# Performance work log

Measured on AMD Instinct MI355X. Metric: run time of the kernel, lower is better.

## Reference

```python
import jax, jax.numpy as jnp
import numpy as np


def _mha(q, k, v, num_heads):
    # q,k,v: [B, L, C] -> multi-head attention, scale = 1/sqrt(head_dim)
    B, Lq, C = q.shape
    Lk = k.shape[1]
    d = C // num_heads
    qh = q.reshape(B, Lq, num_heads, d)
    kh = k.reshape(B, Lk, num_heads, d)
    vh = v.reshape(B, Lk, num_heads, d)
    scale = 1.0 / jnp.sqrt(jnp.asarray(d, q.dtype))
    scores = jnp.einsum('blhd,bmhd->bhlm', qh, kh) * scale
    probs = jax.nn.softmax(scores, axis=-1)
    out = jnp.einsum('bhlm,bmhd->blhd', probs, vh)
    return out.reshape(B, Lq, C)


def setup_inputs() -> dict:
    key = jax.random.key(0)
    ks = jax.random.split(key, 9)
    b, n, f, l, C = 1, 4, 8, 256, 320
    s = 0.02
    return {
        'hidden_states': jax.random.normal(ks[0], (b * n * f, l, C), jnp.float32),
        'Wq': jax.random.normal(ks[1], (C, C), jnp.float32) * s,
        'Wk': jax.random.normal(ks[2], (C, C), jnp.float32) * s,
        'Wv': jax.random.normal(ks[3], (C, C), jnp.float32) * s,
        'Wo': jax.random.normal(ks[4], (C, C), jnp.float32) * s,
        'bo': jnp.zeros((C,), jnp.float32),
        'Wq_i2v': jax.random.normal(ks[5], (C, C), jnp.float32) * s,
        'Wo_i2v': jax.random.normal(ks[6], (C, C), jnp.float32) * s,
        'bo_i2v': jnp.zeros((C,), jnp.float32),
        'num_heads': 8,
        'num_views': 4,
        'num_frames': 8,
    }


def reference(hidden_states, Wq, Wk, Wv, Wo, bo, Wq_i2v, Wo_i2v, bo_i2v,
              num_heads, num_views, num_frames):
    BNF, l, C = hidden_states.shape
    n, f = num_views, num_frames
    b = BNF // (n * f)
    # '(b n f) l c -> (b f) (n l) c'
    h = hidden_states.reshape(b, n, f, l, C).transpose(0, 2, 1, 3, 4).reshape(b * f, n * l, C)
    L = n * l

    q = h @ Wq
    k = h @ Wk
    v = h @ Wv

    # first-frame KV broadcast across all frames within the same b
    k_first = jnp.broadcast_to(k.reshape(b, f, L, C)[:, 0:1], (b, f, L, C)).reshape(b * f, L, C)
    v_first = jnp.broadcast_to(v.reshape(b, f, L, C)[:, 0:1], (b, f, L, C)).reshape(b * f, L, C)

    base = _mha(q, k, v, num_heads)

    q_i2v = h @ Wq_i2v
    i2v = _mha(q_i2v, k_first, v_first, num_heads)
    i2v = i2v @ Wo_i2v + bo_i2v

    out = (base + i2v) @ Wo + bo

    # '(b f) (n l) c -> (b n f) l c'
    out = out.reshape(b, f, n, l, C).transpose(0, 2, 1, 3, 4).reshape(b * n * f, l, C)
    return out
```

## Files before the change

kernel.cpp:

```cpp
#include <hip/hip_runtime.h>

#define MROWS 8192
#define CDIM  320
#define QPAD  512

typedef __attribute__((ext_vector_type(8))) short bf16x8;
typedef __attribute__((ext_vector_type(4))) float f32x4;

__device__ __forceinline__ unsigned bfbits(float x) {
  union { float f; unsigned u; } a; a.f = x;
  return a.u + 0x8000u;
}
__device__ __forceinline__ unsigned pack2bf(float a, float b) {
  return (bfbits(a) >> 16) | (bfbits(b) & 0xffff0000u);
}
__device__ __forceinline__ void splitbf(float x, short& hi, short& lo) {
  unsigned hu = bfbits(x) & 0xffff0000u;
  union { unsigned u; float f; } h; h.u = hu;
  hi = (short)(hu >> 16);
  lo = (short)(bfbits(x - h.f) >> 16);
}

__device__ __forceinline__ int swizzle_row(int r) {
  int ff = r >> 10;
  int t  = r & 1023;
  int nn = t >> 8;
  int ll = t & 255;
  return nn * 2048 + ff * 256 + ll;
}

__global__ __launch_bounds__(256) void wc_kernel(
    const float* __restrict__ Woi, const float* __restrict__ Wo,
    float* __restrict__ Wc)
{
  const int r0 = blockIdx.x * 64, c0 = blockIdx.y * 64;
  __shared__ float As[64][36];
  __shared__ float Bs[32][68];
  const int tid = threadIdx.x, tx = tid & 15, ty = tid >> 4;
  float acc[4][4] = {};

  const int ra = tid >> 3, kq = (tid & 7) * 4;
  const int kb = tid >> 4, cq = (tid & 15) * 4;

  for (int k0 = 0; k0 < 320; k0 += 32) {
    float4 a1 = *(const float4*)(Woi + (size_t)(r0 + ra) * 320 + k0 + kq);
    float4 a2 = *(const float4*)(Woi + (size_t)(r0 + ra + 32) * 320 + k0 + kq);
    float4 b1 = *(const float4*)(Wo + (size_t)(k0 + kb) * 320 + c0 + cq);
    float4 b2 = *(const float4*)(Wo + (size_t)(k0 + kb + 16) * 320 + c0 + cq);
    __syncthreads();
    *(float4*)&As[ra][kq] = a1;
    *(float4*)&As[ra + 32][kq] = a2;
    *(float4*)&Bs[kb][cq] = b1;
    *(float4*)&Bs[kb + 16][cq] = b2;
    __syncthreads();
    #pragma unroll
    for (int kk = 0; kk < 32; ++kk) {
      float4 bv = *(const float4*)&Bs[kk][tx * 4];
      #pragma unroll
      for (int i = 0; i < 4; ++i) {
        float a = As[ty * 4 + i][kk];
        acc[i][0] = fmaf(a, bv.x, acc[i][0]);
        acc[i][1] = fmaf(a, bv.y, acc[i][1]);
        acc[i][2] = fmaf(a, bv.z, acc[i][2]);
        acc[i][3] = fmaf(a, bv.w, acc[i][3]);
      }
    }
  }
  #pragma unroll
  for (int i = 0; i < 4; ++i) {
    float4 v = make_float4(acc[i][0], acc[i][1], acc[i][2], acc[i][3]);
    *(float4*)(Wc + (size_t)(r0 + ty * 4 + i) * 320 + c0 + tx * 4) = v;
  }
}

__global__ __launch_bounds__(256) void pack_kernel(
    const float* __restrict__ hidden,
    const float* __restrict__ Wq, const float* __restrict__ Wk,
    const float* __restrict__ Wv, const float* __restrict__ Wqi,
    const float* __restrict__ Wo, const float* __restrict__ Wc,
    const float* __restrict__ bo, const float* __restrict__ boi,
    short* __restrict__ Ah, short* __restrict__ Al,
    short* __restrict__ WTh, short* __restrict__ WTl,
    short* __restrict__ WFh, short* __restrict__ WFl,
    float* __restrict__ bc,
    short* __restrict__ Qp, short* __restrict__ Kp, short* __restrict__ Qip,
    float qscale)
{
  const int b = blockIdx.x, tid = threadIdx.x;
  if (b < 64) {
    const int r0 = b * 128;
    for (int e = tid; e < 128 * 80; e += 256) {
      int r = e / 80, cq = (e % 80) * 4;
      float4 x = *(const float4*)(hidden + (size_t)swizzle_row(r0 + r) * 320 + cq);
      union { ushort4 v; short s[4]; } h, l;
      splitbf(x.x, h.s[0], l.s[0]); splitbf(x.y, h.s[1], l.s[1]);
      splitbf(x.z, h.s[2], l.s[2]); splitbf(x.w, h.s[3], l.s[3]);
      *(ushort4*)&Ah[(size_t)(r0 + r) * 320 + cq] = h.v;
      *(ushort4*)&Al[(size_t)(r0 + r) * 320 + cq] = l.v;
    }
  } else if (b < 128) {
    const int t2 = b - 64, wi = t2 >> 4, seg = t2 & 15;
    const float* W = wi == 0 ? Wq : wi == 1 ? Wk : wi == 2 ? Wv : Wqi;
    const float s = (wi == 0 || wi == 3) ? qscale : 1.0f;
    short* th = WTh + (size_t)wi * 320 * 320;
    short* tl = WTl + (size_t)wi * 320 * 320;
    for (int e = tid; e < 20 * 320; e += 256) {
      int n = seg * 20 + e / 320, k = e % 320;
      short hi, lo;
      splitbf(W[(size_t)k * 320 + n] * s, hi, lo);
      th[(size_t)n * 320 + k] = hi;
      tl[(size_t)n * 320 + k] = lo;
    }
  } else if (b < 160) {
    const int t2 = b - 128;
    for (int e = tid; e < 10 * 640; e += 256) {
      int n = t2 * 10 + e / 640, k = e % 640;
      float x = (k < 320) ? Wo[(size_t)k * 320 + n] : Wc[(size_t)(k - 320) * 320 + n];
      short hi, lo;
      splitbf(x, hi, lo);
      WFh[(size_t)n * 640 + k] = hi;
      WFl[(size_t)n * 640 + k] = lo;
    }
  } else if (b < 168) {
    const int n = (b - 160) * 40 + tid;
    if (tid < 40) {
      float s = bo[n];
      for (int j = 0; j < 320; ++j) s = fmaf(boi[j], Wo[(size_t)j * 320 + n], s);
      bc[n] = s;
    }
  } else {
    const int bz = b - 168, buf = bz >> 5, seg = bz & 31;
    short* P = buf == 0 ? Qp : buf == 1 ? Kp : Qip;
    const uint4 z = make_uint4(0, 0, 0, 0);
    for (int e = tid; e < 256 * 24; e += 256) {
      int row = (seg << 8) + (e / 24);
      int cc = e % 24, h = cc / 3, c3 = cc % 3;
      *(uint4*)&P[(size_t)row * QPAD + h * 64 + 40 + c3 * 8] = z;
    }
  }
}

__global__ __launch_bounds__(256, 3) void mfma_gemm(
    const short* __restrict__ Ah, const short* __restrict__ Al,
    const short* __restrict__ BTh, const short* __restrict__ BTl,
    int K, int mode,
    short* __restrict__ Qp, short* __restrict__ Kp,
    short* __restrict__ Vt, short* __restrict__ Qip,
    float* __restrict__ Of, const float* __restrict__ bias)
{
  const int tid  = threadIdx.x;
  const int wave = tid >> 6;
  const int lane = tid & 63;
  const int quad = lane >> 4;
  const int l16  = lane & 15;
  const int row0 = blockIdx.x * 128;

  const short *bth, *btl;
  int nbase, wi = 0;
  if (mode == 0) {
    const int ct = blockIdx.y;
    wi = ct / 5;
    bth = BTh + (size_t)wi * 320 * 320;
    btl = BTl + (size_t)wi * 320 * 320;
    nbase = (ct % 5) * 64;
  } else {
    bth = BTh; btl = BTl;
    nbase = blockIdx.y * 64;
  }

  __shared__ short Ash[128][40], Asl[128][40];
  __shared__ short Bsh[64][40],  Bsl[64][40];

  f32x4 acc[2][4];
  #pragma unroll
  for (int mt = 0; mt < 2; ++mt)
    #pragma unroll
    for (int nt = 0; nt < 4; ++nt) acc[mt][nt] = (f32x4){0.f, 0.f, 0.f, 0.f};

  const int ar = tid >> 2, akc = (tid & 3) * 8;
  const int bn = tid >> 2, bkc = (tid & 3) * 8;

  const short* pa_h = Ah + (size_t)(row0 + ar) * K + akc;
  const short* pa_l = Al ? Al + (size_t)(row0 + ar) * K + akc : nullptr;
  const short* pb_h = bth + (size_t)(nbase + bn) * K + bkc;
  const short* pb_l = btl + (size_t)(nbase + bn) * K + bkc;

  for (int k0 = 0; k0 < K; k0 += 32) {
    uint4 ah1 = *(const uint4*)(pa_h + k0);
    uint4 ah2 = *(const uint4*)(pa_h + (size_t)64 * K + k0);
    uint4 al1, al2;
    if (Al) {
      al1 = *(const uint4*)(pa_l + k0);
      al2 = *(const uint4*)(pa_l + (size_t)64 * K + k0);
    }
    uint4 bh = *(const uint4*)(pb_h + k0);
    uint4 bl = *(const uint4*)(pb_l + k0);
    __syncthreads();
    *(uint4*)&Ash[ar][akc]      = ah1;
    *(uint4*)&Ash[ar + 64][akc] = ah2;
    if (Al) {
      *(uint4*)&Asl[ar][akc]      = al1;
      *(uint4*)&Asl[ar + 64][akc] = al2;
    }
    *(uint4*)&Bsh[bn][bkc] = bh;
    *(uint4*)&Bsl[bn][bkc] = bl;
    __syncthreads();

    bf16x8 afh[2], afl[2], bfh[4], bfl[4];
    #pragma unroll
    for (int mt = 0; mt < 2; ++mt) {
      afh[mt] = *(const bf16x8*)&Ash[wave * 32 + mt * 16 + l16][quad * 8];
      if (Al) afl[mt] = *(const bf16x8*)&Asl[wave * 32 + mt * 16 + l16][quad * 8];
    }
    #pragma unroll
    for (int nt = 0; nt < 4; ++nt) {
      bfh[nt] = *(const bf16x8*)&Bsh[nt * 16 + l16][quad * 8];
      bfl[nt] = *(const bf16x8*)&Bsl[nt * 16 + l16][quad * 8];
    }
    #pragma unroll
    for (int mt = 0; mt < 2; ++mt)
      #pragma unroll
      for (int nt = 0; nt < 4; ++nt) {
        acc[mt][nt] = __builtin_amdgcn_mfma_f32_16x16x32_bf16(afh[mt], bfh[nt], acc[mt][nt], 0, 0, 0);
        acc[mt][nt] = __builtin_amdgcn_mfma_f32_16x16x32_bf16(afh[mt], bfl[nt], acc[mt][nt], 0, 0, 0);
        if (Al)
          acc[mt][nt] = __builtin_amdgcn_mfma_f32_16x16x32_bf16(afl[mt], bfh[nt], acc[mt][nt], 0, 0, 0);
      }
  }

  if (mode == 0) {
    if (wi == 2) {
      #pragma unroll
      for (int mt = 0; mt < 2; ++mt)
        #pragma unroll
        for (int nt = 0; nt < 4; ++nt) {
          const int col  = nbase + nt * 16 + l16;
          const int rowb = row0 + wave * 32 + mt * 16 + quad * 4;
          union { ushort4 v; short s[4]; } pk;
          #pragma unroll
          for (int r = 0; r < 4; ++r) pk.s[r] = (short)(bfbits(acc[mt][nt][r]) >> 16);
          *(ushort4*)&Vt[(size_t)col * MROWS + rowb] = pk.v;
        }
    } else {
      short* Op = wi == 0 ? Qp : wi == 1 ? Kp : Qip;
      #pragma unroll
      for (int mt = 0; mt < 2; ++mt)
        #pragma unroll
        for (int nt = 0; nt < 4; ++nt) {
          const int col  = nbase + nt * 16 + l16;
          const int h    = col / 40;
          const int pcol = h * 64 + (col - h * 40);
          const int rowb = row0 + wave * 32 + mt * 16 + quad * 4;
          #pragma unroll
          for (int r = 0; r < 4; ++r)
            Op[(size_t)(rowb + r) * QPAD + pcol] = (short)(bfbits(acc[mt][nt][r]) >> 16);
        }
    }
  } else {
    #pragma unroll
    for (int mt = 0; mt < 2; ++mt)
      #pragma unroll
      for (int nt = 0; nt < 4; ++nt) {
        const int col  = nbase + nt * 16 + l16;
        const int rowb = row0 + wave * 32 + mt * 16 + quad * 4;
        const float bb = bias[col];
        #pragma unroll
        for (int r = 0; r < 4; ++r)
          Of[(size_t)swizzle_row(rowb + r) * CDIM + col] = acc[mt][nt][r] + bb;
      }
  }
}

__global__ __launch_bounds__(64, 2) void attn_kernel(
    const short* __restrict__ Qp, const short* __restrict__ Qip,
    const short* __restrict__ Kp, const short* __restrict__ Vtg,
    short* __restrict__ AOh)
{
  const int qblk = blockIdx.x;
  const int hh   = blockIdx.y;
  const int zz   = blockIdx.z;
  const int var  = zz >> 3;
  const int bf   = zz & 7;
  const int lane = threadIdx.x;
  const int quad = lane >> 4;
  const int l16  = lane & 15;

  const short* Q = var ? Qip : Qp;
  const int kvbase = var ? 0 : (bf << 10);
  const int coff = var * 320 + hh * 40;

  __shared__ short Ps[4][16][72];

  bf16x8 qf0[4], qf1[4];
  #pragma unroll
  for (int qt = 0; qt < 4; ++qt) {
    const short* qp = Q + (size_t)((bf << 10) + (qblk << 6) + (qt << 4) + l16) * QPAD + hh * 64;
    qf0[qt] = *(const bf16x8*)(qp + quad * 8);
    qf1[qt] = *(const bf16x8*)(qp + 32 + quad * 8);
  }

  f32x4 acc[4][3];
  float lsum[4];
  #pragma unroll
  for (int qt = 0; qt < 4; ++qt) {
    lsum[qt] = 0.f;
    #pragma unroll
    for (int t = 0; t < 3; ++t) acc[qt][t] = (f32x4){0.f, 0.f, 0.f, 0.f};
  }

  const short* Kb = Kp + (size_t)kvbase * QPAD + hh * 64;
  const short* Vb = Vtg + (size_t)(hh * 40) * MROWS + kvbase;

  for (int s0 = 0; s0 < 1024; s0 += 64) {
    bf16x8 kb0[4], kb1[4];
    #pragma unroll
    for (int kt = 0; kt < 4; ++kt) {
      const short* kp = Kb + (size_t)(s0 + kt * 16 + l16) * QPAD;
      kb0[kt] = *(const bf16x8*)(kp + quad * 8);
      kb1[kt] = *(const bf16x8*)(kp + 32 + quad * 8);
    }

    #pragma unroll
    for (int qt = 0; qt < 4; ++qt) {
      float ls = 0.f;
      #pragma unroll
      for (int kt = 0; kt < 4; ++kt) {
        f32x4 st = (f32x4){0.f, 0.f, 0.f, 0.f};
        st = __builtin_amdgcn_mfma_f32_16x16x32_bf16(kb0[kt], qf0[qt], st, 0, 0, 0);
        st = __builtin_amdgcn_mfma_f32_16x16x32_bf16(kb1[kt], qf1[qt], st, 0, 0, 0);
        float p0 = __expf(st[0]);
        float p1 = __expf(st[1]);
        float p2 = __expf(st[2]);
        float p3 = __expf(st[3]);
        ls += (p0 + p1) + (p2 + p3);
        uint2 pk;
        pk.x = pack2bf(p0, p1);
        pk.y = pack2bf(p2, p3);
        *(uint2*)&Ps[qt][l16][kt * 16 + quad * 4] = pk;
      }
      lsum[qt] += ls;
    }

    asm volatile("s_waitcnt lgkmcnt(0)" ::: "memory");

    bf16x8 vf[2][3];
    #pragma unroll
    for (int kh = 0; kh < 2; ++kh)
      #pragma unroll
      for (int t = 0; t < 3; ++t)
        vf[kh][t] = *(const bf16x8*)(Vb + (size_t)(t * 16 + l16) * MROWS + s0 + kh * 32 + quad * 8);

    #pragma unroll
    for (int qt = 0; qt < 4; ++qt) {
      bf16x8 pa0 = *(const bf16x8*)&Ps[qt][l16][quad * 8];
      bf16x8 pa1 = *(const bf16x8*)&Ps[qt][l16][32 + quad * 8];
      #pragma unroll
      for (int t = 0; t < 3; ++t) {
        acc[qt][t] = __builtin_amdgcn_mfma_f32_16x16x32_bf16(pa0, vf[0][t], acc[qt][t], 0, 0, 0);
        acc[qt][t] = __builtin_amdgcn_mfma_f32_16x16x32_bf16(pa1, vf[1][t], acc[qt][t], 0, 0, 0);
      }
    }
  }

  #pragma unroll
  for (int qt = 0; qt < 4; ++qt) {
    float li = lsum[qt];
    li += __shfl_xor(li, 16);
    li += __shfl_xor(li, 32);
    float inv = 1.f / li;
    float invr[4];
    #pragma unroll
    for (int r = 0; r < 4; ++r) invr[r] = __shfl(inv, quad * 4 + r, 64);

    const int baserow = (bf << 10) + (qblk << 6) + (qt << 4) + quad * 4;
    #pragma unroll
    for (int t = 0; t < 3; ++t) {
      int dcol = t * 16 + l16;
      if (dcol < 40) {
        short* op = AOh + (size_t)baserow * 640 + coff + dcol;
        #pragma unroll
        for (int r = 0; r < 4; ++r)
          op[(size_t)r * 640] = (short)(bfbits(acc[qt][t][r] * invr[r]) >> 16);
      }
    }
  }
}

extern "C" void kernel_launch(void* const* d_in, const int* in_sizes, int n_in,
                              void* d_out, int out_size, void* d_ws, size_t ws_size,
                              hipStream_t stream) {
  const float* hidden  = (const float*)d_in[0];
  const float* Wq      = (const float*)d_in[1];
  const float* Wk      = (const float*)d_in[2];
  const float* Wv      = (const float*)d_in[3];
  const float* Wo      = (const float*)d_in[4];
  const float* bo      = (const float*)d_in[5];
  const float* Wq_i2v  = (const float*)d_in[6];
  const float* Wo_i2v  = (const float*)d_in[7];
  const float* bo_i2v  = (const float*)d_in[8];
  float* out = (float*)d_out;

  const size_t SZ  = (size_t)MROWS * CDIM;
  const size_t SZP = (size_t)MROWS * QPAD;
  short* Ah  = (short*)d_ws;
  short* Al  = Ah + SZ;
  short* AOh = Ah;
  short* Qp  = Al + SZ;
  short* Kp  = Qp + SZP;
  short* Qip = Kp + SZP;
  short* Vt  = Qip + SZP;
  short* WTh = Vt + (size_t)328 * MROWS;
  short* WTl = WTh + 409600;
  short* WFh = WTl + 409600;
  short* WFl = WFh + 204800;
  float* Wc  = (float*)(WFl + 204800);
  float* bc  = Wc + 102400;

  const float qscale = 0.15811388300841898f;

  wc_kernel<<<dim3(5, 5), 256, 0, stream>>>(Wo_i2v, Wo, Wc);

  pack_kernel<<<dim3(264), 256, 0, stream>>>(
      hidden, Wq, Wk, Wv, Wq_i2v, Wo, Wc, bo, bo_i2v,
      Ah, Al, WTh, WTl, WFh, WFl, bc, Qp, Kp, Qip, qscale);

  mfma_gemm<<<dim3(64, 20), 256, 0, stream>>>(
      Ah, Al, WTh, WTl, 320, 0, Qp, Kp, Vt, Qip, nullptr, nullptr);

  attn_kernel<<<dim3(16, 8, 16), 64, 0, stream>>>(Qp, Qip, Kp, Vt, AOh);

  mfma_gemm<<<dim3(64, 5), 256, 0, stream>>>(
      AOh, nullptr, WFh, WFl, 640, 1, nullptr, nullptr, nullptr, nullptr, out, bc);
}
```

Before: 229.2 us.

## Share K/V tiles in LDS across four waves per attention block

The attention kernel moves from one wave per 64-query block to four waves per 128-query block, each wave handling 32 queries. K and V tiles are staged cooperatively into shared memory once per key step and read by all four waves, instead of each wave loading them from global memory. The K rows are permuted through gbase so the reordered key columns line up with how P is packed. This adds two barriers per iteration and halves the number of blocks, which lowers latency hiding per block and makes the row permutation a correctness risk.

New measurement: 219.8 us. 4.1% less time.

```diff
diff --git a/kernel.cpp b/kernel.cpp
--- a/kernel.cpp
+++ b/kernel.cpp
@@ -271,7 +271,7 @@
   }
 }
 
-__global__ __launch_bounds__(64, 2) void attn_kernel(
+__global__ __launch_bounds__(256, 4) void attn_kernel(
     const short* __restrict__ Qp, const short* __restrict__ Qip,
     const short* __restrict__ Kp, const short* __restrict__ Vtg,
     short* __restrict__ AOh)
@@ -281,7 +281,9 @@
   const int zz   = blockIdx.z;
   const int var  = zz >> 3;
   const int bf   = zz & 7;
-  const int lane = threadIdx.x;
+  const int tid  = threadIdx.x;
+  const int wave = tid >> 6;
+  const int lane = tid & 63;
   const int quad = lane >> 4;
   const int l16  = lane & 15;
 
@@ -289,39 +291,63 @@
   const int kvbase = var ? 0 : (bf << 10);
   const int coff = var * 320 + hh * 40;
 
-  __shared__ short Ps[4][16][72];
-
-  bf16x8 qf0[4], qf1[4];
+  __shared__ short Ks[64][80];
+  __shared__ short Vt[48][72];
+  __shared__ short Ps[4][2][16][72];
+
+  if (tid < 64) {
+    *(uint4*)&Vt[40 + (tid >> 3)][(tid & 7) * 8] = make_uint4(0, 0, 0, 0);
+  }
+
+  bf16x8 qf0[2], qf1[2];
   #pragma unroll
-  for (int qt = 0; qt < 4; ++qt) {
-    const short* qp = Q + (size_t)((bf << 10) + (qblk << 6) + (qt << 4) + l16) * QPAD + hh * 64;
+  for (int qt = 0; qt < 2; ++qt) {
+    const short* qp = Q + (size_t)((bf << 10) + (qblk << 7) + (wave << 5) + (qt << 4) + l16) * QPAD + hh * 64;
     qf0[qt] = *(const bf16x8*)(qp + quad * 8);
     qf1[qt] = *(const bf16x8*)(qp + 32 + quad * 8);
   }
 
-  f32x4 acc[4][3];
-  float lsum[4];
+  f32x4 acc[2][3];
+  float lsum[2] = {0.f, 0.f};
   #pragma unroll
-  for (int qt = 0; qt < 4; ++qt) {
-    lsum[qt] = 0.f;
+  for (int qt = 0; qt < 2; ++qt)
     #pragma unroll
     for (int t = 0; t < 3; ++t) acc[qt][t] = (f32x4){0.f, 0.f, 0.f, 0.f};
-  }
 
   const short* Kb = Kp + (size_t)kvbase * QPAD + hh * 64;
   const short* Vb = Vtg + (size_t)(hh * 40) * MROWS + kvbase;
 
+  const int gbase = (l16 & 3) + ((l16 >> 2) << 4);
+
   for (int s0 = 0; s0 < 1024; s0 += 64) {
+    __syncthreads();
+    #pragma unroll
+    for (int pass = 0; pass < 4; ++pass) {
+      int u = tid + (pass << 8);
+      if (u < 512) {
+        int key = u >> 3, c = u & 7;
+        *(uint4*)&Ks[key][c * 8] =
+            *(const uint4*)(Kb + (size_t)(s0 + key) * QPAD + c * 8);
+      } else if (u < 832) {
+        int v = u - 512;
+        int dcol = v >> 3, ch = v & 7;
+        *(uint4*)&Vt[dcol][ch * 8] =
+            *(const uint4*)(Vb + (size_t)dcol * MROWS + s0 + ch * 8);
+      }
+    }
+    __syncthreads();
+
     bf16x8 kb0[4], kb1[4];
     #pragma unroll
     for (int kt = 0; kt < 4; ++kt) {
-      const short* kp = Kb + (size_t)(s0 + kt * 16 + l16) * QPAD;
-      kb0[kt] = *(const bf16x8*)(kp + quad * 8);
-      kb1[kt] = *(const bf16x8*)(kp + 32 + quad * 8);
-    }
-
-    #pragma unroll
-    for (int qt = 0; qt < 4; ++qt) {
+      const short* kr = &Ks[gbase + 4 * kt][quad * 8];
+      kb0[kt] = *(const bf16x8*)kr;
+      kb1[kt] = *(const bf16x8*)(kr + 32);
+    }
+
+    #pragma unroll
+    for (int qt = 0; qt < 2; ++qt) {
+      unsigned pbuf[8];
       float ls = 0.f;
       #pragma unroll
       for (int kt = 0; kt < 4; ++kt) {
@@ -333,37 +359,30 @@
         float p2 = __expf(st[2]);
         float p3 = __expf(st[3]);
         ls += (p0 + p1) + (p2 + p3);
-        uint2 pk;
-        pk.x = pack2bf(p0, p1);
-        pk.y = pack2bf(p2, p3);
-        *(uint2*)&Ps[qt][l16][kt * 16 + quad * 4] = pk;
+        pbuf[kt * 2]     = pack2bf(p0, p1);
+        pbuf[kt * 2 + 1] = pack2bf(p2, p3);
       }
       lsum[qt] += ls;
-    }
-
-    asm volatile("s_waitcnt lgkmcnt(0)" ::: "memory");
-
-    bf16x8 vf[2][3];
-    #pragma unroll
-    for (int kh = 0; kh < 2; ++kh)
-      #pragma unroll
-      for (int t = 0; t < 3; ++t)
-        vf[kh][t] = *(const bf16x8*)(Vb + (size_t)(t * 16 + l16) * MROWS + s0 + kh * 32 + quad * 8);
-
-    #pragma unroll
-    for (int qt = 0; qt < 4; ++qt) {
-      bf16x8 pa0 = *(const bf16x8*)&Ps[qt][l16][quad * 8];
-      bf16x8 pa1 = *(const bf16x8*)&Ps[qt][l16][32 + quad * 8];
+
+      *(uint4*)&Ps[wave][qt][l16][quad * 16]     = *(uint4*)&pbuf[0];
+      *(uint4*)&Ps[wave][qt][l16][quad * 16 + 8] = *(uint4*)&pbuf[4];
+
+      asm volatile("s_waitcnt lgkmcnt(0)" ::: "memory");
+
+      bf16x8 pa0 = *(const bf16x8*)&Ps[wave][qt][l16][quad * 8];
+      bf16x8 pa1 = *(const bf16x8*)&Ps[wave][qt][l16][32 + quad * 8];
       #pragma unroll
       for (int t = 0; t < 3; ++t) {
-        acc[qt][t] = __builtin_amdgcn_mfma_f32_16x16x32_bf16(pa0, vf[0][t], acc[qt][t], 0, 0, 0);
-        acc[qt][t] = __builtin_amdgcn_mfma_f32_16x16x32_bf16(pa1, vf[1][t], acc[qt][t], 0, 0, 0);
+        bf16x8 v0 = *(const bf16x8*)&Vt[t * 16 + l16][quad * 8];
+        bf16x8 v1 = *(const bf16x8*)&Vt[t * 16 + l16][32 + quad * 8];
+        acc[qt][t] = __builtin_amdgcn_mfma_f32_16x16x32_bf16(pa0, v0, acc[qt][t], 0, 0, 0);
+        acc[qt][t] = __builtin_amdgcn_mfma_f32_16x16x32_bf16(pa1, v1, acc[qt][t], 0, 0, 0);
       }
     }
   }
 
   #pragma unroll
-  for (int qt = 0; qt < 4; ++qt) {
+  for (int qt = 0; qt < 2; ++qt) {
     float li = lsum[qt];
     li += __shfl_xor(li, 16);
     li += __shfl_xor(li, 32);
@@ -372,7 +391,7 @@
     #pragma unroll
     for (int r = 0; r < 4; ++r) invr[r] = __shfl(inv, quad * 4 + r, 64);
 
-    const int baserow = (bf << 10) + (qblk << 6) + (qt << 4) + quad * 4;
+    const int baserow = (bf << 10) + (qblk << 7) + (wave << 5) + (qt << 4) + quad * 4;
     #pragma unroll
     for (int t = 0; t < 3; ++t) {
       int dcol = t * 16 + l16;
@@ -427,7 +446,7 @@
   mfma_gemm<<<dim3(64, 20), 256, 0, stream>>>(
       Ah, Al, WTh, WTl, 320, 0, Qp, Kp, Vt, Qip, nullptr, nullptr);
 
-  attn_kernel<<<dim3(16, 8, 16), 64, 0, stream>>>(Qp, Qip, Kp, Vt, AOh);
+  attn_kernel<<<dim3(8, 8, 16), 256, 0, stream>>>(Qp, Qip, Kp, Vt, AOh);
 
   mfma_gemm<<<dim3(64, 5), 256, 0, stream>>>(
       AOh, nullptr, WFh, WFl, 640, 1, nullptr, nullptr, nullptr, nullptr, out, bc);
```
